# Optimization experiments

Hardware: AMD Instinct MI355X
Metric: run time of the kernel (lower is better)

Reference implementation:

```python
import jax, jax.numpy as jnp
import numpy as np

N = 20000   # atoms
E = 320000  # edges (avg degree 16)
H = 128     # hidden_channels / num_filters
G = 128     # num_gaussians
L = 4       # num_interactions
B = 200     # molecules
V = 80      # _MAX_ATOM_TYPE
CUT = 5.0
LOG2 = float(np.log(2.0))


def setup_inputs() -> dict:
    key = jax.random.key(0)
    ks = jax.random.split(key, 20)
    s = 0.05
    pos = jax.random.uniform(ks[0], (N, 3), dtype=jnp.float32) * 2.5  # dists < 5 = cutoff
    z = jax.random.randint(ks[1], (N,), 0, V)
    batch = jnp.sort(jax.random.randint(ks[2], (N,), 0, B))
    row = jax.random.randint(ks[3], (E,), 0, N)
    off = jax.random.randint(ks[4], (E,), 1, N)
    col = (row + off) % N  # guarantee row != col (no zero distances)
    edge_index = jnp.stack([row, col], axis=0)
    return {
        'pos': pos, 'z': z, 'batch': batch, 'edge_index': edge_index,
        'emb': jax.random.normal(ks[5], (V, H), jnp.float32) * s,
        'mlp_w1': jax.random.normal(ks[6], (L, G, H), jnp.float32) * s,
        'mlp_b1': jnp.zeros((L, H), jnp.float32),
        'mlp_w2': jax.random.normal(ks[7], (L, H, H), jnp.float32) * s,
        'mlp_b2': jnp.zeros((L, H), jnp.float32),
        'conv_lin1_w': jax.random.normal(ks[8], (L, H, H), jnp.float32) * s,
        'conv_lin2_w': jax.random.normal(ks[9], (L, H, H), jnp.float32) * s,
        'conv_lin2_b': jnp.zeros((L, H), jnp.float32),
        'blk_lin_w': jax.random.normal(ks[10], (L, H, H), jnp.float32) * s,
        'blk_lin_b': jnp.zeros((L, H), jnp.float32),
        'head_w1': jax.random.normal(ks[11], (H, H // 2), jnp.float32) * s,
        'head_b1': jnp.zeros((H // 2,), jnp.float32),
        'head_w2': jax.random.normal(ks[12], (H // 2, 1), jnp.float32) * s,
        'head_b2': jnp.zeros((1,), jnp.float32),
    }


def _ssp(x):  # ShiftedSoftplus
    return jax.nn.softplus(x) - LOG2


def _energy(pos, emb, mlp_w1, mlp_b1, mlp_w2, mlp_b2, conv_lin1_w, conv_lin2_w,
            conv_lin2_b, blk_lin_w, blk_lin_b, head_w1, head_b1, head_w2, head_b2,
            z, batch, edge_index):
    row, col = edge_index[0], edge_index[1]
    diff = pos[row] - pos[col]
    d = jnp.sqrt(jnp.sum(diff * diff, axis=-1))  # [E]
    # GaussianSmearing(0, cutoff, G)
    offset = jnp.linspace(0.0, CUT, G, dtype=pos.dtype)
    coeff = -0.5 / (offset[1] - offset[0]) ** 2
    edge_attr = jnp.exp(coeff * (d[:, None] - offset[None, :]) ** 2)  # [E,G]
    Ccut = 0.5 * (jnp.cos(d * jnp.pi / CUT) + 1.0)  # [E]
    h = emb[z]  # [N,H]
    for i in range(L):
        # per-edge filter MLP * cosine cutoff
        W = _ssp(edge_attr @ mlp_w1[i] + mlp_b1[i]) @ mlp_w2[i] + mlp_b2[i]
        W = W * Ccut[:, None]  # [E,H]
        hx = h @ conv_lin1_w[i]  # lin1, no bias
        msg = hx[row] * W  # gather x_j * filter
        agg = jax.ops.segment_sum(msg, col, num_segments=N)  # scatter-add
        v = agg @ conv_lin2_w[i] + conv_lin2_b[i]
        h = h + (_ssp(v) @ blk_lin_w[i] + blk_lin_b[i])  # residual InteractionBlock
    hh = _ssp(h @ head_w1 + head_b1) @ head_w2 + head_b2  # [N,1]
    return jax.ops.segment_sum(hh[:, 0], batch, num_segments=B)  # [B]


def reference(pos, z, batch, edge_index, emb, mlp_w1, mlp_b1, mlp_w2, mlp_b2,
              conv_lin1_w, conv_lin2_w, conv_lin2_b, blk_lin_w, blk_lin_b,
              head_w1, head_b1, head_w2, head_b2):
    args = (emb, mlp_w1, mlp_b1, mlp_w2, mlp_b2, conv_lin1_w, conv_lin2_w,
            conv_lin2_b, blk_lin_w, blk_lin_b, head_w1, head_b1, head_w2, head_b2)
    out = _energy(pos, *args, z, batch, edge_index)
    # forces = -d(sum(energy))/d(pos), matching torch.autograd.grad with ones grad_outputs
    forces = -jax.grad(lambda p: jnp.sum(_energy(p, *args, z, batch, edge_index)))(pos)
    return out, forces
```

## Files before the change

kernel.cpp:

```cpp
#include <hip/hip_runtime.h>

#define HD 128

constexpr int N_ATOMS = 20000;
constexpr int N_EDGES = 320000;
constexpr int NLAY   = 4;
constexpr int NMOL   = 200;
constexpr float FCUT  = 5.0f;
constexpr float DELTA = FCUT / 127.0f;
constexpr float GCOEFF = -0.5f / (DELTA * DELTA);
constexpr float PI_F  = 3.14159265358979323846f;
constexpr float LN2F  = 0.6931471805599453f;

typedef unsigned short u16;
typedef __attribute__((ext_vector_type(8))) short short8v;
typedef __attribute__((ext_vector_type(4))) float f32x4;

__device__ __forceinline__ float sspf(float x) {
  return fmaxf(x, 0.0f) + log1pf(expf(-fabsf(x))) - LN2F;
}
__device__ __forceinline__ float sigmf(float x) {
  return 1.0f / (1.0f + expf(-x));
}

__device__ __forceinline__ unsigned bfpack(float a, float b) {
  unsigned ua = __float_as_uint(a);
  unsigned ub = __float_as_uint(b);
  ua = (ua + 0x7FFFu + ((ua >> 16) & 1u)) >> 16;
  ub = (ub + 0x7FFFu + ((ub >> 16) & 1u)) >> 16;
  return (ub << 16) | ua;
}
__device__ __forceinline__ float bflo(unsigned p) { return __uint_as_float(p << 16); }
__device__ __forceinline__ float bfhi(unsigned p) { return __uint_as_float(p & 0xFFFF0000u); }
__device__ __forceinline__ u16 f2bf(float x) {
  unsigned u = __float_as_uint(x);
  u = (u + 0x7FFFu + ((u >> 16) & 1u)) >> 16;
  return (u16)u;
}
__device__ __forceinline__ float bf2f(u16 b) { return __uint_as_float((unsigned)b << 16); }

__device__ __forceinline__ unsigned packhl(float s) {
  unsigned hs = __float_as_uint(s) & 0xffff0000u;
  float lo = s - __uint_as_float(hs);
  return hs | (__float_as_uint(lo) >> 16);
}

__device__ __forceinline__ unsigned hpair_f32(unsigned a, unsigned b, unsigned& lopair) {
  unsigned ha = a & 0xffff0000u, hb = b & 0xffff0000u;
  float la = __uint_as_float(a) - __uint_as_float(ha);
  float lb = __uint_as_float(b) - __uint_as_float(hb);
  lopair = (__float_as_uint(lb) & 0xffff0000u) | (__float_as_uint(la) >> 16);
  return hb | (ha >> 16);
}


__global__ __launch_bounds__(256) void h0_k(
    const float* __restrict__ emb, const int* __restrict__ z,
    float* __restrict__ h0)
{
  int i = blockIdx.x * 256 + threadIdx.x;
  if (i >= N_ATOMS * HD) return;
  int n = i >> 7, k = i & 127;
  h0[i] = emb[z[n] * HD + k];
}

__global__ __launch_bounds__(256) void wprep_k(
    const float* __restrict__ l1, const float* __restrict__ l2,
    const float* __restrict__ bw, const float* __restrict__ mw1,
    const float* __restrict__ mw2,
    u16* __restrict__ wt, u16* __restrict__ wp, u16* __restrict__ mt)
{
  int i = blockIdx.x * 256 + threadIdx.x;
  if (i >= NLAY * 5 * HD * HD) return;
  int e = i & (HD * HD - 1);
  int wl = i >> 14;
  int wsel = wl % 5;
  int lay = wl / 5;
  const float* W;
  if      (wsel == 0) W = l1;
  else if (wsel == 1) W = l2;
  else if (wsel == 2) W = bw;
  else if (wsel == 3) W = mw1;
  else                W = mw2;
  W += (size_t)lay * HD * HD;
  u16 b = f2bf(W[e]);
  int k = e >> 7, n = e & 127;
  if (wsel < 3) {
    size_t base = (size_t)(lay * 3 + wsel) << 14;
    wp[base + e] = b;
    wt[base + (size_t)n * HD + k] = b;
  } else {
    size_t base = (size_t)(lay * 2 + (wsel - 3)) << 14;
    mt[base + (size_t)n * HD + k] = b;
  }
}

__global__ __launch_bounds__(256) void histboth_k(
    const int* __restrict__ row, const int* __restrict__ col,
    int* __restrict__ cntR, int* __restrict__ cntC)
{
  int e = blockIdx.x * 256 + threadIdx.x;
  if (e >= N_EDGES) return;
  atomicAdd(&cntC[col[e]], 1);
  atomicAdd(&cntR[row[e]], 1);
}

__global__ __launch_bounds__(256) void scan2_k(
    const int* __restrict__ cnt0, const int* __restrict__ cnt1,
    int* __restrict__ cptr, int* __restrict__ rptr,
    int* __restrict__ cur0, int* __restrict__ cur1,
    int* __restrict__ binc, int* __restrict__ binr)
{
  constexpr int CH = 80;
  __shared__ int part[256];
  __shared__ int lh[256];
  const int* cnt = blockIdx.x == 0 ? cnt0 : cnt1;
  int* ptr = blockIdx.x == 0 ? cptr : rptr;
  int* cur = blockIdx.x == 0 ? cur0 : cur1;
  int* bin = blockIdx.x == 0 ? binc : binr;
  int t = threadIdx.x;
  lh[t] = 0;
  int base = t * CH;
  int v[CH];
  if (base + CH <= N_ATOMS) {
#pragma unroll
    for (int i = 0; i < CH / 4; i++) {
      int4 q = *(const int4*)(cnt + base + i * 4);
      v[4*i+0] = q.x; v[4*i+1] = q.y; v[4*i+2] = q.z; v[4*i+3] = q.w;
    }
  } else {
#pragma unroll
    for (int i = 0; i < CH; i++)
      v[i] = (base + i < N_ATOMS) ? cnt[base + i] : 0;
  }
  __syncthreads();
#pragma unroll
  for (int i = 0; i < CH; i++)
    if (base + i < N_ATOMS) atomicAdd(&lh[255 - min(v[i], 255)], 1);
  int s = 0;
#pragma unroll
  for (int i = 0; i < CH; i++) s += v[i];
  part[t] = s;
  __syncthreads();
  bin[t] = lh[t];
  for (int off = 1; off < 256; off <<= 1) {
    int u = (t >= off) ? part[t - off] : 0;
    __syncthreads();
    part[t] += u;
    __syncthreads();
  }
  int run = part[t] - s;
#pragma unroll
  for (int i = 0; i < CH; i++) {
    int idx = base + i;
    if (idx < N_ATOMS) { ptr[idx] = run; cur[idx] = run; }
    else if (idx == N_ATOMS) ptr[idx] = run;
    run += v[i];
  }
}

__global__ __launch_bounds__(256) void scatboth_k(
    const float* __restrict__ pos, const int* __restrict__ row,
    const int* __restrict__ col, int* __restrict__ cur0,
    int* __restrict__ cur1, uint2* __restrict__ cpk2,
    uint2* __restrict__ rpk2, float* __restrict__ cdist,
    float* __restrict__ rdist, int* __restrict__ cslot, float inv_h)
{
  int e = blockIdx.x * 256 + threadIdx.x;
  if (e >= N_EDGES) return;
  int r = row[e], c = col[e];
  float dx = pos[3*r+0] - pos[3*c+0];
  float dy = pos[3*r+1] - pos[3*c+1];
  float dz = pos[3*r+2] - pos[3*c+2];
  float d = sqrtf(dx*dx + dy*dy + dz*dz);
  float fi = d * inv_h;
  int i0 = (int)fi;
  float t = fi - (float)i0;
  unsigned pk = (unsigned)c | ((unsigned)i0 << 16);
  unsigned tu = __float_as_uint(t);
  int pr = atomicAdd(&cur1[r], 1);
  rpk2[pr] = make_uint2(pk, tu);
  rdist[pr] = d;
  int pc = atomicAdd(&cur0[c], 1);
  cpk2[pc] = make_uint2((unsigned)r | ((unsigned)i0 << 16), tu);
  cdist[pc] = d;
  cslot[pc] = pr;
}

__global__ __launch_bounds__(256) void dscan_k(
    int* __restrict__ binc, int* __restrict__ binr)
{
  int* bin = blockIdx.x == 0 ? binc : binr;
  __shared__ int sh[256];
  int t = threadIdx.x;
  int v = bin[t];
  sh[t] = v;
  __syncthreads();
  for (int off = 1; off < 256; off <<= 1) {
    int u = (t >= off) ? sh[t - off] : 0;
    __syncthreads();
    sh[t] += u;
    __syncthreads();
  }
  bin[t] = sh[t] - v;
}

__global__ __launch_bounds__(256) void dscat_k(
    const int* __restrict__ cptr, const int* __restrict__ rptr,
    int* __restrict__ binc, int* __restrict__ binr,
    int* __restrict__ permc, int* __restrict__ permr)
{
  __shared__ int lhc[256], lhr[256], lbc[256], lbr[256];
  int t = threadIdx.x;
  lhc[t] = 0; lhr[t] = 0;
  __syncthreads();
  int a = blockIdx.x * 256 + t;
  int bc = 0, br = 0, rc = 0, rr = 0;
  bool valid = a < N_ATOMS;
  if (valid) {
    int dc = cptr[a+1] - cptr[a];
    int dr = rptr[a+1] - rptr[a];
    bc = 255 - min(dc, 255);
    br = 255 - min(dr, 255);
    rc = atomicAdd(&lhc[bc], 1);
    rr = atomicAdd(&lhr[br], 1);
  }
  __syncthreads();
  if (lhc[t] > 0) lbc[t] = atomicAdd(&binc[t], lhc[t]);
  if (lhr[t] > 0) lbr[t] = atomicAdd(&binr[t], lhr[t]);
  __syncthreads();
  if (valid) {
    permc[lbc[bc] + rc] = a;
    permr[lbr[br] + rr] = a;
  }
}

__global__ __launch_bounds__(256) void nodeA_k(
    float* __restrict__ A, float* __restrict__ dA, int nnode, float hstep)
{
  int i = blockIdx.x * 256 + threadIdx.x;
  if (i >= nnode * HD) return;
  int node = i >> 7, g = i & 127;
  float d = (float)node * hstep;
  float t = d - (float)g * DELTA;
  float a = expf(GCOEFF * t * t);
  A[i] = a;
  dA[i] = a * 2.0f * GCOEFF * t;
}

__global__ __launch_bounds__(256) void nodeact_k(
    const float* __restrict__ t1, const float* __restrict__ u,
    float* __restrict__ s, float* __restrict__ sp, int total)
{
  int i = blockIdx.x * 256 + threadIdx.x;
  if (i >= total) return;
  float x = t1[i];
  s[i] = sspf(x);
  sp[i] = sigmf(x) * u[i];
}

__global__ __launch_bounds__(256) void nodecomb_k(
    const float* __restrict__ P0, const float* __restrict__ D0,
    unsigned* __restrict__ T, int nnode, float hstep)
{
  int i = blockIdx.x * 256 + threadIdx.x;
  int total = NLAY * nnode * HD;
  if (i >= total) return;
  int rem = i % (nnode * HD);
  int node = rem >> 7;
  float d = (float)node * hstep;
  float C  = 0.5f * cosf(d * (PI_F / FCUT)) + 0.5f;
  float Cp = -0.5f * sinf(d * (PI_F / FCUT)) * (PI_F / FCUT);
  float p = P0[i], q = D0[i];
  T[i] = bfpack(p * C, q * C + p * Cp);
}

__device__ __forceinline__ void wave_mm(
    const float* __restrict__ Av, const u16* __restrict__ Bt,
    int m0, int wbase, int lc, int lg, int mclamp, f32x4 acc[2])
{
  short8v bfr[4][2];
#pragma unroll
  for (int ks = 0; ks < 4; ++ks)
#pragma unroll
    for (int nt = 0; nt < 2; ++nt)
      bfr[ks][nt] = *(const short8v*)(Bt + (size_t)(wbase + nt*16 + lc) * HD + ks*32 + lg*8);
  int ar = m0 + lc;
  if (ar > mclamp) ar = mclamp;
  f32x4 z = {0.f, 0.f, 0.f, 0.f};
  acc[0] = z; acc[1] = z;
#pragma unroll
  for (int ks = 0; ks < 4; ++ks) {
    const float* p = Av + (size_t)ar * HD + ks*32 + lg*8;
    uint4 u0 = *(const uint4*)p;
    uint4 u1 = *(const uint4*)(p + 4);
    unsigned p0l, p1l, p2l, p3l;
    unsigned p0h = hpair_f32(u0.x, u0.y, p0l);
    unsigned p1h = hpair_f32(u0.z, u0.w, p1l);
    unsigned p2h = hpair_f32(u1.x, u1.y, p2l);
    unsigned p3h = hpair_f32(u1.z, u1.w, p3l);
    uint4 hv = make_uint4(p0h, p1h, p2h, p3h);
    uint4 lv = make_uint4(p0l, p1l, p2l, p3l);
    short8v ah = *(short8v*)&hv, al = *(short8v*)&lv;
    acc[0] = __builtin_amdgcn_mfma_f32_16x16x32_bf16(ah, bfr[ks][0], acc[0], 0, 0, 0);
    acc[1] = __builtin_amdgcn_mfma_f32_16x16x32_bf16(ah, bfr[ks][1], acc[1], 0, 0, 0);
    acc[0] = __builtin_amdgcn_mfma_f32_16x16x32_bf16(al, bfr[ks][0], acc[0], 0, 0, 0);
    acc[1] = __builtin_amdgcn_mfma_f32_16x16x32_bf16(al, bfr[ks][1], acc[1], 0, 0, 0);
  }
}

__device__ __forceinline__ void wave_mm_lds(
    const unsigned (*__restrict__ Sl)[132], const u16* __restrict__ Bt,
    int wbase, int lc, int lg, f32x4 acc[2])
{
  short8v bfr[4][2];
#pragma unroll
  for (int ks = 0; ks < 4; ++ks)
#pragma unroll
    for (int nt = 0; nt < 2; ++nt)
      bfr[ks][nt] = *(const short8v*)(Bt + (size_t)(wbase + nt*16 + lc) * HD + ks*32 + lg*8);
  f32x4 z = {0.f, 0.f, 0.f, 0.f};
  acc[0] = z; acc[1] = z;
#pragma unroll
  for (int ks = 0; ks < 4; ++ks) {
    uint4 u0 = *(const uint4*)&Sl[lc][ks*32 + lg*8];
    uint4 u1 = *(const uint4*)&Sl[lc][ks*32 + lg*8 + 4];
    uint4 hv = make_uint4(
      (u0.y & 0xffff0000u) | (u0.x >> 16),
      (u0.w & 0xffff0000u) | (u0.z >> 16),
      (u1.y & 0xffff0000u) | (u1.x >> 16),
      (u1.w & 0xffff0000u) | (u1.z >> 16));
    uint4 lv = make_uint4(
      (u0.y << 16) | (u0.x & 0xffffu),
      (u0.w << 16) | (u0.z & 0xffffu),
      (u1.y << 16) | (u1.x & 0xffffu),
      (u1.w << 16) | (u1.z & 0xffffu));
    short8v ah = *(short8v*)&hv, al = *(short8v*)&lv;
    acc[0] = __builtin_amdgcn_mfma_f32_16x16x32_bf16(ah, bfr[ks][0], acc[0], 0, 0, 0);
    acc[1] = __builtin_amdgcn_mfma_f32_16x16x32_bf16(ah, bfr[ks][1], acc[1], 0, 0, 0);
    acc[0] = __builtin_amdgcn_mfma_f32_16x16x32_bf16(al, bfr[ks][0], acc[0], 0, 0, 0);
    acc[1] = __builtin_amdgcn_mfma_f32_16x16x32_bf16(al, bfr[ks][1], acc[1], 0, 0, 0);
  }
}

__global__ __launch_bounds__(256) void nmm_hx_k(
    const float* __restrict__ h, const u16* __restrict__ Bt,
    u16* __restrict__ hx, int M)
{
  int t = threadIdx.x, lane = t & 63;
  int lc = lane & 15, lg = lane >> 4;
  int wbase = (t >> 6) * 32;
  int m0 = blockIdx.x * 16;
  f32x4 acc[2];
  wave_mm(h, Bt, m0, wbase, lc, lg, M - 1, acc);
#pragma unroll
  for (int nt = 0; nt < 2; ++nt) {
    int ccol = wbase + nt*16 + lc;
#pragma unroll
    for (int j = 0; j < 4; ++j) {
      int grow = m0 + lg*4 + j;
      if (grow < M) hx[(size_t)grow * HD + ccol] = f2bf(acc[nt][j]);
    }
  }
}

__global__ __launch_bounds__(256) void nmm_bwdT_k(
    const float* __restrict__ A, const u16* __restrict__ Bp,
    const float* __restrict__ addin, float* __restrict__ C, int M)
{
  int t = threadIdx.x, lane = t & 63;
  int lc = lane & 15, lg = lane >> 4;
  int wbase = (t >> 6) * 32;
  int m0 = blockIdx.x * 16;
  f32x4 acc[2];
  wave_mm(A, Bp, m0, wbase, lc, lg, M - 1, acc);
#pragma unroll
  for (int nt = 0; nt < 2; ++nt) {
    int ccol = wbase + nt*16 + lc;
#pragma unroll
    for (int j = 0; j < 4; ++j) {
      int grow = m0 + lg*4 + j;
      if (grow < M)
        C[(size_t)grow * HD + ccol] = acc[nt][j] + addin[(size_t)grow * HD + ccol];
    }
  }
}

__global__ __launch_bounds__(256) void ftail_f_k(
    const float* __restrict__ agg, const u16* __restrict__ l2t,
    const float* __restrict__ l2b, const u16* __restrict__ bwt,
    const float* __restrict__ bb, const float* __restrict__ h,
    u16* __restrict__ svb, float* __restrict__ hout,
    const u16* __restrict__ l1n, u16* __restrict__ hxn, int M)
{
  __shared__ unsigned Sl[16][132];
  int t = threadIdx.x, lane = t & 63;
  int lc = lane & 15, lg = lane >> 4;
  int wbase = (t >> 6) * 32;
  int m0 = blockIdx.x * 16;
  f32x4 acc[2];
  wave_mm(agg, l2t, m0, wbase, lc, lg, M - 1, acc);
#pragma unroll
  for (int nt = 0; nt < 2; ++nt) {
    int ccol = wbase + nt*16 + lc;
    float bv = l2b[ccol];
#pragma unroll
    for (int j = 0; j < 4; ++j) {
      int lrow = lg*4 + j;
      int grow = m0 + lrow;
      float s = 0.0f;
      if (grow < M) {
        float x = acc[nt][j] + bv;
        svb[(size_t)grow * HD + ccol] = f2bf(sigmf(x));
        s = sspf(x);
      }
      Sl[lrow][ccol] = packhl(s);
    }
  }
  __syncthreads();
  wave_mm_lds(Sl, bwt, wbase, lc, lg, acc);

  float ho[2][4];
#pragma unroll
  for (int nt = 0; nt < 2; ++nt) {
    int ccol = wbase + nt*16 + lc;
    float bv = bb[ccol];
#pragma unroll
    for (int j = 0; j < 4; ++j) {
      int grow = m0 + lg*4 + j;
      float x = 0.0f;
      if (grow < M) {
        x = acc[nt][j] + bv + h[(size_t)grow * HD + ccol];
        hout[(size_t)grow * HD + ccol] = x;
      }
      ho[nt][j] = x;
    }
  }
  if (l1n) {
    __syncthreads();
#pragma unroll
    for (int nt = 0; nt < 2; ++nt) {
      int ccol = wbase + nt*16 + lc;
#pragma unroll
      for (int j = 0; j < 4; ++j)
        Sl[lg*4 + j][ccol] = packhl(ho[nt][j]);
    }
    __syncthreads();
    wave_mm_lds(Sl, l1n, wbase, lc, lg, acc);
#pragma unroll
    for (int nt = 0; nt < 2; ++nt) {
      int ccol = wbase + nt*16 + lc;
#pragma unroll
      for (int j = 0; j < 4; ++j) {
        int grow = m0 + lg*4 + j;
        if (grow < M) hxn[(size_t)grow * HD + ccol] = f2bf(acc[nt][j]);
      }
    }
  }
}

__global__ __launch_bounds__(256) void bhead_f_k(
    const float* __restrict__ g, const u16* __restrict__ bwp,
    const u16* __restrict__ svb, const u16* __restrict__ l2p,
    u16* __restrict__ dagg, int M)
{
  __shared__ unsigned Sl[16][132];
  int t = threadIdx.x, lane = t & 63;
  int lc = lane & 15, lg = lane >> 4;
  int wbase = (t >> 6) * 32;
  int m0 = blockIdx.x * 16;
  f32x4 acc[2];
  wave_mm(g, bwp, m0, wbase, lc, lg, M - 1, acc);
#pragma unroll
  for (int nt = 0; nt < 2; ++nt) {
    int ccol = wbase + nt*16 + lc;
#pragma unroll
    for (int j = 0; j < 4; ++j) {
      int lrow = lg*4 + j;
      int grow = m0 + lrow;
      float dv = 0.0f;
      if (grow < M)
        dv = acc[nt][j] * bf2f(svb[(size_t)grow * HD + ccol]);
      Sl[lrow][ccol] = packhl(dv);
    }
  }
  __syncthreads();
  wave_mm_lds(Sl, l2p, wbase, lc, lg, acc);
#pragma unroll
  for (int nt = 0; nt < 2; ++nt) {
    int ccol = wbase + nt*16 + lc;
#pragma unroll
    for (int j = 0; j < 4; ++j) {
      int grow = m0 + lg*4 + j;
      if (grow < M) dagg[(size_t)grow * HD + ccol] = f2bf(acc[nt][j]);
    }
  }
}

__global__ __launch_bounds__(256) void tblmm2_k(
    const float* __restrict__ A0, const float* __restrict__ A1, size_t astride,
    const u16* __restrict__ Bt, size_t bstride,
    const float* __restrict__ bias0, size_t biasstride,
    float* __restrict__ C0, float* __restrict__ C1, size_t cstride, int M)
{
  int l = blockIdx.y;
  int zz = blockIdx.z;
  const float* A = (zz ? A1 : A0) + (size_t)l * astride;
  const u16* B = Bt + (size_t)l * bstride;
  const float* bias = zz ? nullptr : (bias0 ? bias0 + (size_t)l * biasstride : nullptr);
  float* C = (zz ? C1 : C0) + (size_t)l * cstride;
  int t = threadIdx.x, lane = t & 63;
  int lc = lane & 15, lg = lane >> 4;
  int wbase = (t >> 6) * 32;
  int m0 = blockIdx.x * 16;
  f32x4 acc[2];
  wave_mm(A, B, m0, wbase, lc, lg, M - 1, acc);
#pragma unroll
  for (int nt = 0; nt < 2; ++nt) {
    int ccol = wbase + nt*16 + lc;
    float bv = bias ? bias[ccol] : 0.0f;
#pragma unroll
    for (int j = 0; j < 4; ++j) {
      int grow = m0 + lg*4 + j;
      if (grow < M) C[(size_t)grow * HD + ccol] = acc[nt][j] + bv;
    }
  }
}

__global__ __launch_bounds__(256) void gath_fwd_k(
    const int* __restrict__ perm, const int* __restrict__ cptr,
    const uint2* __restrict__ cpk2, const unsigned* __restrict__ T,
    const unsigned* __restrict__ hx, float* __restrict__ agg, float hstep)
{
  int ai = blockIdx.x * 4 + (threadIdx.x >> 6);
  if (ai >= N_ATOMS) return;
  int a = perm[ai];
  int half = (threadIdx.x >> 5) & 1;
  int l32 = threadIdx.x & 31;
  int ch = l32 * 4;
  int beg = cptr[a], end = cptr[a + 1];
  float s0 = 0.f, s1 = 0.f, s2 = 0.f, s3 = 0.f;
#pragma unroll 2
  for (int j = beg + half; j < end; j += 2) {
    uint2 pk2 = cpk2[j];
    float t = __uint_as_float(pk2.y);
    int other = pk2.x & 0xffffu;
    float t2 = t * t, t3 = t2 * t;
    float cx = 2.f*t3 - 3.f*t2 + 1.f;
    float cy = (t3 - 2.f*t2 + t) * hstep;
    float cz = 3.f*t2 - 2.f*t3;
    float cw = (t3 - t2) * hstep;
    const unsigned* tp = T + (size_t)(pk2.x >> 16) * HD + ch;
    uint4 q0 = *(const uint4*)(tp);
    uint4 q1 = *(const uint4*)(tp + HD);
    uint2 hp = *(const uint2*)(hx + (size_t)other * 64 + l32 * 2);
    float v0 = cx*bflo(q0.x) + cy*bfhi(q0.x) + cz*bflo(q1.x) + cw*bfhi(q1.x);
    float v1 = cx*bflo(q0.y) + cy*bfhi(q0.y) + cz*bflo(q1.y) + cw*bfhi(q1.y);
    float v2 = cx*bflo(q0.z) + cy*bfhi(q0.z) + cz*bflo(q1.z) + cw*bfhi(q1.z);
    float v3 = cx*bflo(q0.w) + cy*bfhi(q0.w) + cz*bflo(q1.w) + cw*bfhi(q1.w);
    s0 = fmaf(bflo(hp.x), v0, s0);
    s1 = fmaf(bfhi(hp.x), v1, s1);
    s2 = fmaf(bflo(hp.y), v2, s2);
    s3 = fmaf(bfhi(hp.y), v3, s3);
  }
  s0 += __shfl_xor(s0, 32, 64);
  s1 += __shfl_xor(s1, 32, 64);
  s2 += __shfl_xor(s2, 32, 64);
  s3 += __shfl_xor(s3, 32, 64);
  if (half == 0)
    *(float4*)(agg + (size_t)a * HD + ch) = make_float4(s0, s1, s2, s3);
}

__global__ __launch_bounds__(256) void gath_bwd_k(
    const int* __restrict__ perm, const int* __restrict__ rptr,
    const uint2* __restrict__ rpk2, const unsigned* __restrict__ T,
    const unsigned* __restrict__ dagg, const unsigned* __restrict__ hx,
    float* __restrict__ dhx, float* __restrict__ ddslot, int accum,
    float hstep, float inv_h)
{
  int ai = blockIdx.x * 4 + (threadIdx.x >> 6);
  if (ai >= N_ATOMS) return;
  int a = perm[ai];
  int half = (threadIdx.x >> 5) & 1;
  int l32 = threadIdx.x & 31;
  int ch = l32 * 4;
  int beg = rptr[a], end = rptr[a + 1];
  uint2 hp = *(const uint2*)(hx + (size_t)a * 64 + l32 * 2);
  float h0 = bflo(hp.x), h1 = bfhi(hp.x), h2 = bflo(hp.y), h3 = bfhi(hp.y);
  float s0 = 0.f, s1 = 0.f, s2 = 0.f, s3 = 0.f;
#pragma unroll 2
  for (int j = beg + half; j < end; j += 2) {
    uint2 pk2 = rpk2[j];
    float t = __uint_as_float(pk2.y);
    int other = pk2.x & 0xffffu;
    float t2 = t * t, t3 = t2 * t;
    float cax = 2.f*t3 - 3.f*t2 + 1.f;
    float cay = (t3 - 2.f*t2 + t) * hstep;
    float caz = 3.f*t2 - 2.f*t3;
    float caw = (t3 - t2) * hstep;
    float cbx = (6.f*t2 - 6.f*t) * inv_h;
    float cby = 3.f*t2 - 4.f*t + 1.f;
    float cbz = -cbx;
    float cbw = 3.f*t2 - 2.f*t;
    const unsigned* tp = T + (size_t)(pk2.x >> 16) * HD + ch;
    uint4 q0 = *(const uint4*)(tp);
    uint4 q1 = *(const uint4*)(tp + HD);
    uint2 dp = *(const uint2*)(dagg + (size_t)other * 64 + l32 * 2);
    float da0 = bflo(dp.x), da1 = bfhi(dp.x), da2 = bflo(dp.y), da3 = bfhi(dp.y);
    float x0l = bflo(q0.x), x0h = bfhi(q0.x), y0l = bflo(q1.x), y0h = bfhi(q1.x);
    float x1l = bflo(q0.y), x1h = bfhi(q0.y), y1l = bflo(q1.y), y1h = bfhi(q1.y);
    float x2l = bflo(q0.z), x2h = bfhi(q0.z), y2l = bflo(q1.z), y2h = bfhi(q1.z);
    float x3l = bflo(q0.w), x3h = bfhi(q0.w), y3l = bflo(q1.w), y3h = bfhi(q1.w);
    float v0 = cax*x0l + cay*x0h + caz*y0l + caw*y0h;
    float v1 = cax*x1l + cay*x1h + caz*y1l + caw*y1h;
    float v2 = cax*x2l + cay*x2h + caz*y2l + caw*y2h;
    float v3 = cax*x3l + cay*x3h + caz*y3l + caw*y3h;
    float g0 = cbx*x0l + cby*x0h + cbz*y0l + cbw*y0h;
    float g1 = cbx*x1l + cby*x1h + cbz*y1l + cbw*y1h;
    float g2 = cbx*x2l + cby*x2h + cbz*y2l + cbw*y2h;
    float g3 = cbx*x3l + cby*x3h + cbz*y3l + cbw*y3h;
    s0 = fmaf(da0, v0, s0);
    s1 = fmaf(da1, v1, s1);
    s2 = fmaf(da2, v2, s2);
    s3 = fmaf(da3, v3, s3);
    float dot = da0*h0*g0 + da1*h1*g1 + da2*h2*g2 + da3*h3*g3;
#pragma unroll
    for (int off = 16; off > 0; off >>= 1) dot += __shfl_down(dot, off, 32);
    if (l32 == 0) ddslot[j] = accum ? (ddslot[j] + dot) : dot;
  }
  s0 += __shfl_xor(s0, 32, 64);
  s1 += __shfl_xor(s1, 32, 64);
  s2 += __shfl_xor(s2, 32, 64);
  s3 += __shfl_xor(s3, 32, 64);
  if (half == 0)
    *(float4*)(dhx + (size_t)a * HD + ch) = make_float4(s0, s1, s2, s3);
}

__global__ __launch_bounds__(256) void headf_k(
    const float* __restrict__ h4, const float* __restrict__ hw1,
    const float* __restrict__ hb1, const float* __restrict__ hw2,
    const float* __restrict__ hb2, float* __restrict__ ea,
    float* __restrict__ gh)
{
  __shared__ float As[16][68];
  __shared__ float Bs[16][132];
  __shared__ float Ss[64][68];
  __shared__ float red[64][17];
  int t = threadIdx.x;
  int tx = t & 15, ty = t >> 4;
  int m0 = blockIdx.x * 64;

  float acc4[4][4];
#pragma unroll
  for (int r = 0; r < 4; r++)
#pragma unroll
    for (int c = 0; c < 4; c++) acc4[r][c] = 0.0f;

  for (int k0 = 0; k0 < HD; k0 += 16) {
    {
      int rrow = t >> 2;
      int kg = (t & 3) * 4;
      int gm = m0 + rrow;
      float4 av = make_float4(0.f, 0.f, 0.f, 0.f);
      if (gm < N_ATOMS) av = *(const float4*)(h4 + (size_t)gm * HD + k0 + kg);
      As[kg+0][rrow] = av.x; As[kg+1][rrow] = av.y;
      As[kg+2][rrow] = av.z; As[kg+3][rrow] = av.w;
    }
    if (t < 256) {
      int kk = t >> 4;
      int n4 = (t & 15) * 4;
      float4 bv = *(const float4*)(hw1 + (size_t)(k0 + kk) * 64 + n4);
      *(float4*)&Bs[kk][n4] = bv;
    }
    __syncthreads();
#pragma unroll
    for (int kk = 0; kk < 16; kk++) {
      float a[4], b[4];
#pragma unroll
      for (int r = 0; r < 4; r++) a[r] = As[kk][ty * 4 + r];
#pragma unroll
      for (int c = 0; c < 4; c++) b[c] = Bs[kk][tx * 4 + c];
#pragma unroll
      for (int r = 0; r < 4; r++)
#pragma unroll
        for (int c = 0; c < 4; c++) acc4[r][c] = fmaf(a[r], b[c], acc4[r][c]);
    }
    __syncthreads();
  }

  {
    int n0 = tx * 4;
    float b1v[4], w2v[4];
#pragma unroll
    for (int c = 0; c < 4; c++) { b1v[c] = hb1[n0 + c]; w2v[c] = hw2[n0 + c]; }
#pragma unroll
    for (int r = 0; r < 4; r++) {
      int lr = ty * 4 + r;
      float p = 0.0f;
#pragma unroll
      for (int c = 0; c < 4; c++) {
        float x = acc4[r][c] + b1v[c];
        p += sspf(x) * w2v[c];
        Ss[lr][n0 + c] = sigmf(x) * w2v[c];
      }
      red[lr][tx] = p;
    }
  }
  __syncthreads();
  if (t < 64) {
    int gm = m0 + t;
    if (gm < N_ATOMS) {
      float s = hb2[0];
#pragma unroll
      for (int j = 0; j < 16; j++) s += red[t][j];
      ea[gm] = s;
    }
  }

  float acc[4][8];
#pragma unroll
  for (int r = 0; r < 4; r++)
#pragma unroll
    for (int c = 0; c < 8; c++) acc[r][c] = 0.0f;

  for (int j0 = 0; j0 < 64; j0 += 16) {
#pragma unroll
    for (int it = 0; it < 2; it++) {
      int idx = t + it * 256;
      int n = idx >> 2;
      int jg = (idx & 3) * 4;
      float4 bv = *(const float4*)(hw1 + (size_t)n * 64 + j0 + jg);
      Bs[jg+0][n] = bv.x; Bs[jg+1][n] = bv.y;
      Bs[jg+2][n] = bv.z; Bs[jg+3][n] = bv.w;
    }
    __syncthreads();
#pragma unroll
    for (int kk = 0; kk < 16; kk++) {
      float a[4], b[8];
#pragma unroll
      for (int r = 0; r < 4; r++) a[r] = Ss[ty * 4 + r][j0 + kk];
#pragma unroll
      for (int c = 0; c < 8; c++) b[c] = Bs[kk][tx * 8 + c];
#pragma unroll
      for (int r = 0; r < 4; r++)
#pragma unroll
        for (int c = 0; c < 8; c++) acc[r][c] = fmaf(a[r], b[c], acc[r][c]);
    }
    __syncthreads();
  }

  int n0 = tx * 8;
#pragma unroll
  for (int r = 0; r < 4; r++) {
    int gm = m0 + ty * 4 + r;
    if (gm >= N_ATOMS) continue;
    *(float4*)(gh + (size_t)gm * HD + n0)     = *(float4*)&acc[r][0];
    *(float4*)(gh + (size_t)gm * HD + n0 + 4) = *(float4*)&acc[r][4];
  }
}

__global__ __launch_bounds__(64) void ered_k(
    const int* __restrict__ batch, const float* __restrict__ ea,
    float* __restrict__ energy)
{
  int m = blockIdx.x;
  int lo = 0, hi = N_ATOMS;
  while (lo < hi) { int mid = (lo + hi) >> 1; if (batch[mid] < m) lo = mid + 1; else hi = mid; }
  int beg = lo;
  lo = beg; hi = N_ATOMS;
  while (lo < hi) { int mid = (lo + hi) >> 1; if (batch[mid] < m + 1) lo = mid + 1; else hi = mid; }
  int end = lo;
  float s = 0.0f;
  for (int i = beg + threadIdx.x; i < end; i += 64) s += ea[i];
#pragma unroll
  for (int off = 32; off > 0; off >>= 1) s += __shfl_down(s, off, 64);
  if (threadIdx.x == 0) energy[m] = s;
}

__global__ __launch_bounds__(256) void forceg_k(
    const int* __restrict__ rptr, const uint2* __restrict__ rpk2,
    const float* __restrict__ rdist,
    const int* __restrict__ cptr, const uint2* __restrict__ cpk2,
    const float* __restrict__ cdist, const int* __restrict__ cslot,
    const float* __restrict__ ddslot, const float* __restrict__ pos,
    float* __restrict__ force)
{
  int idx = blockIdx.x * 256 + threadIdx.x;
  int a = idx >> 3;
  int g = idx & 7;
  if (a >= N_ATOMS) return;
  float px = pos[3*a+0], py = pos[3*a+1], pz = pos[3*a+2];
  float fx = 0.f, fy = 0.f, fz = 0.f;
  int beg = rptr[a], end = rptr[a+1];
  for (int j = beg + g; j < end; j += 8) {
    int o = rpk2[j].x & 0xffffu;
    float w = ddslot[j] / rdist[j];
    fx -= w * (px - pos[3*o+0]);
    fy -= w * (py - pos[3*o+1]);
    fz -= w * (pz - pos[3*o+2]);
  }
  beg = cptr[a]; end = cptr[a+1];
  for (int j = beg + g; j < end; j += 8) {
    int o = cpk2[j].x & 0xffffu;
    float w = ddslot[cslot[j]] / cdist[j];
    fx -= w * (px - pos[3*o+0]);
    fy -= w * (py - pos[3*o+1]);
    fz -= w * (pz - pos[3*o+2]);
  }
#pragma unroll
  for (int off = 4; off > 0; off >>= 1) {
    fx += __shfl_down(fx, off, 8);
    fy += __shfl_down(fy, off, 8);
    fz += __shfl_down(fz, off, 8);
  }
  if (g == 0) {
    force[3*a+0] = fx;
    force[3*a+1] = fy;
    force[3*a+2] = fz;
  }
}

static inline int nblk(int m) { return (m + 63) / 64; }

extern "C" void kernel_launch(void* const* d_in, const int* in_sizes, int n_in,
                              void* d_out, int out_size, void* d_ws, size_t ws_size,
                              hipStream_t stream)
{
  const float* pos   = (const float*)d_in[0];
  const int*   z     = (const int*)d_in[1];
  const int*   batch = (const int*)d_in[2];
  const int*   eidx  = (const int*)d_in[3];
  const float* emb   = (const float*)d_in[4];
  const float* mlp_w1 = (const float*)d_in[5];
  const float* mlp_b1 = (const float*)d_in[6];
  const float* mlp_w2 = (const float*)d_in[7];
  const float* mlp_b2 = (const float*)d_in[8];
  const float* lin1_w = (const float*)d_in[9];
  const float* lin2_w = (const float*)d_in[10];
  const float* lin2_b = (const float*)d_in[11];
  const float* blk_w  = (const float*)d_in[12];
  const float* blk_b  = (const float*)d_in[13];
  const float* hw1 = (const float*)d_in[14];
  const float* hb1 = (const float*)d_in[15];
  const float* hw2 = (const float*)d_in[16];
  const float* hb2 = (const float*)d_in[17];

  float* out = (float*)d_out;
  float* ws  = (float*)d_ws;

  const int* row = eidx;
  const int* col = eidx + N_EDGES;

  const size_t NH = (size_t)N_ATOMS * HD;
  size_t o = 0;
  float* ddslot = ws + o; o += N_EDGES;
  int* cptr = (int*)(ws + o); o += N_ATOMS + 1;
  int* rptr = (int*)(ws + o); o += N_ATOMS + 1;
  int* cnt0 = (int*)(ws + o); o += N_ATOMS;
  int* cnt1 = (int*)(ws + o); o += N_ATOMS;
  int* binc = (int*)(ws + o); o += 256;
  int* binr = (int*)(ws + o); o += 256;
  int* cur0 = (int*)(ws + o); o += N_ATOMS;
  int* cur1 = (int*)(ws + o); o += N_ATOMS;
  int* permc = (int*)(ws + o); o += N_ATOMS;
  int* permr = (int*)(ws + o); o += N_ATOMS;
  int* cslot = (int*)(ws + o); o += N_EDGES;
  float* cdist = ws + o; o += N_EDGES;
  float* rdist = ws + o; o += N_EDGES;
  o = (o + 1) & ~(size_t)1;
  uint2* cpk2 = (uint2*)(ws + o); o += (size_t)2 * N_EDGES;
  uint2* rpk2 = (uint2*)(ws + o); o += (size_t)2 * N_EDGES;
  u16* wt = (u16*)(ws + o); o += (size_t)NLAY * 3 * HD * HD / 2;
  u16* wp = (u16*)(ws + o); o += (size_t)NLAY * 3 * HD * HD / 2;
  u16* mt = (u16*)(ws + o); o += (size_t)NLAY * 2 * HD * HD / 2;
  float* hxb[4];
  for (int i = 0; i < 4; i++) { hxb[i] = ws + o; o += NH / 2; }
  float* svb[4];
  for (int i = 0; i < 4; i++) { svb[i] = ws + o; o += NH / 2; }
  float* hA  = ws + o; o += NH;
  float* hB  = ws + o; o += NH;
  float* agg = ws + o; o += NH;
  float* g0b = ws + o; o += NH;
  float* g1b = ws + o; o += NH;
  float* dgb = ws + o; o += NH / 2;

  int NT = 1024;
  while (NT > 128) {
    size_t need = o + (size_t)NLAY * (NT + 1) * HD;
    if (need * sizeof(float) <= ws_size) break;
    NT >>= 1;
  }
  const int NN = NT + 1;
  const float hstep = FCUT / (float)NT;
  const float inv_h = (float)NT / FCUT;
  unsigned* T = (unsigned*)(ws + o); o += (size_t)NLAY * NN * HD;

  const int EB = (N_EDGES + 255) / 256;
  const int ABK = (N_ATOMS + 255) / 256;

  hipMemsetAsync(cnt0, 0, 2 * N_ATOMS * sizeof(int), stream);

  wprep_k<<<(NLAY * 5 * HD * HD + 255) / 256, 256, 0, stream>>>(
      lin1_w, lin2_w, blk_w, mlp_w1, mlp_w2, wt, wp, mt);

  histboth_k<<<EB, 256, 0, stream>>>(row, col, cnt1, cnt0);
  scan2_k<<<2, 256, 0, stream>>>(cnt0, cnt1, cptr, rptr, cur0, cur1, binc, binr);
  scatboth_k<<<EB, 256, 0, stream>>>(pos, row, col, cur0, cur1, cpk2, rpk2,
                                     cdist, rdist, cslot, inv_h);

  dscan_k<<<2, 256, 0, stream>>>(binc, binr);
  dscat_k<<<ABK, 256, 0, stream>>>(cptr, rptr, binc, binr, permc, permr);

  {
    const size_t LNH = (size_t)NN * HD;
    float* Anode  = agg;
    float* dAnode = agg + LNH;
    float* t1 = dgb;
    float* u  = g0b;
    float* s  = g1b;
    float* sp = hA;
    nodeA_k<<<((int)LNH + 255) / 256, 256, 0, stream>>>(Anode, dAnode, NN, hstep);
    dim3 gB16((NN + 15) / 16, NLAY, 2);
    tblmm2_k<<<gB16, 256, 0, stream>>>(Anode, dAnode, 0, mt, 32768,
                                       mlp_b1, HD, t1, u, LNH, NN);
    int tot = (int)(NLAY * LNH);
    nodeact_k<<<(tot + 255) / 256, 256, 0, stream>>>(t1, u, s, sp, tot);
    float* P0 = dgb;
    float* D0 = g0b;
    tblmm2_k<<<gB16, 256, 0, stream>>>(s, sp, LNH, mt + 16384, 32768,
                                       mlp_b2, HD, P0, D0, LNH, NN);
    nodecomb_k<<<(tot + 255) / 256, 256, 0, stream>>>(P0, D0, T, NN, hstep);
  }

  h0_k<<<(N_ATOMS * HD + 255) / 256, 256, 0, stream>>>(emb, z, hA);

  const int AB = (N_ATOMS + 3) / 4;
  const int GB = nblk(N_ATOMS);
  const int NB16 = (N_ATOMS + 15) / 16;

  float* hcur = hA;
  float* hnxt = hB;
  nmm_hx_k<<<NB16, 256, 0, stream>>>(hcur, wt, (u16*)hxb[0], N_ATOMS);
  for (int i = 0; i < NLAY; i++) {
    const u16* l2t = wt + ((size_t)(i*3 + 1) << 14);
    const u16* bwt = wt + ((size_t)(i*3 + 2) << 14);
    const u16* l1n = (i < NLAY - 1) ? wt + ((size_t)((i+1)*3 + 0) << 14) : nullptr;
    u16* hxn = (i < NLAY - 1) ? (u16*)hxb[i+1] : nullptr;
    const float* l2bi = lin2_b + (size_t)i * HD;
    const float* bbi  = blk_b + (size_t)i * HD;
    const unsigned* Tl = T + (size_t)i * NN * HD;

    gath_fwd_k<<<AB, 256, 0, stream>>>(permc, cptr, cpk2, Tl,
                                       (const unsigned*)hxb[i], agg, hstep);
    ftail_f_k<<<NB16, 256, 0, stream>>>(agg, l2t, l2bi, bwt, bbi, hcur,
                                        (u16*)svb[i], hnxt, l1n, hxn, N_ATOMS);
    float* tmp = hcur; hcur = hnxt; hnxt = tmp;
  }

  float* ea = dgb;
  headf_k<<<GB, 256, 0, stream>>>(hcur, hw1, hb1, hw2, hb2, ea, g0b);
  ered_k<<<NMOL, 64, 0, stream>>>(batch, ea, out);

  float* gcur = g0b;
  float* gnxt = g1b;
  for (int i = NLAY - 1; i >= 0; i--) {
    const u16* l1p = wp + ((size_t)(i*3 + 0) << 14);
    const u16* l2p = wp + ((size_t)(i*3 + 1) << 14);
    const u16* bwp = wp + ((size_t)(i*3 + 2) << 14);
    const unsigned* Tl = T + (size_t)i * NN * HD;

    bhead_f_k<<<NB16, 256, 0, stream>>>(gcur, bwp, (const u16*)svb[i], l2p,
                                        (u16*)dgb, N_ATOMS);
    gath_bwd_k<<<AB, 256, 0, stream>>>(permr, rptr, rpk2, Tl,
                                       (const unsigned*)dgb,
                                       (const unsigned*)hxb[i], agg, ddslot,
                                       i != NLAY - 1, hstep, inv_h);
    if (i > 0) {
      nmm_bwdT_k<<<NB16, 256, 0, stream>>>(agg, l1p, gcur, gnxt, N_ATOMS);
      float* tmp = gcur; gcur = gnxt; gnxt = tmp;
    }
  }

  forceg_k<<<(N_ATOMS * 8 + 255) / 256, 256, 0, stream>>>(
      rptr, rpk2, rdist, cptr, cpk2, cdist, cslot, ddslot, pos, out + NMOL);
}
```

Before: 768.1 us.

## Fuse backward lin1-transpose GEMM into next block head kernel; skip unused dhx

The separate nmm_bwdT kernel, which computed the hidden gradient from the aggregated dhx, is folded into the next layer's bhead kernel. That kernel now does the lin1-transpose GEMM plus residual add, stages the result in LDS and runs the blk-lin GEMM from there, which removes a launch and a global round trip of the gradient. The layer-0 gather-backward also skips the unused dhx accumulation and its spline coefficients, since no downstream consumer needs it. In exchange the fused kernel adds an extra GEMM stage and syncs per block, and still writes gout when a later layer needs it.

Measured after the change: 763.3 us. About the same (-0.6%).

```diff
diff --git a/kernel.cpp b/kernel.cpp
--- a/kernel.cpp
+++ b/kernel.cpp
@@ -364,28 +364,6 @@
   }
 }
 
-__global__ __launch_bounds__(256) void nmm_bwdT_k(
-    const float* __restrict__ A, const u16* __restrict__ Bp,
-    const float* __restrict__ addin, float* __restrict__ C, int M)
-{
-  int t = threadIdx.x, lane = t & 63;
-  int lc = lane & 15, lg = lane >> 4;
-  int wbase = (t >> 6) * 32;
-  int m0 = blockIdx.x * 16;
-  f32x4 acc[2];
-  wave_mm(A, Bp, m0, wbase, lc, lg, M - 1, acc);
-#pragma unroll
-  for (int nt = 0; nt < 2; ++nt) {
-    int ccol = wbase + nt*16 + lc;
-#pragma unroll
-    for (int j = 0; j < 4; ++j) {
-      int grow = m0 + lg*4 + j;
-      if (grow < M)
-        C[(size_t)grow * HD + ccol] = acc[nt][j] + addin[(size_t)grow * HD + ccol];
-    }
-  }
-}
-
 __global__ __launch_bounds__(256) void ftail_f_k(
     const float* __restrict__ agg, const u16* __restrict__ l2t,
     const float* __restrict__ l2b, const u16* __restrict__ bwt,
@@ -459,10 +437,12 @@
   }
 }
 
-__global__ __launch_bounds__(256) void bhead_f_k(
-    const float* __restrict__ g, const u16* __restrict__ bwp,
-    const u16* __restrict__ svb, const u16* __restrict__ l2p,
-    u16* __restrict__ dagg, int M)
+__global__ __launch_bounds__(256) void bhead2_f_k(
+    const float* __restrict__ aggprev, const u16* __restrict__ l1prev,
+    const float* __restrict__ gadd, const float* __restrict__ gdirect,
+    const u16* __restrict__ bwp, const u16* __restrict__ svb,
+    const u16* __restrict__ l2p, u16* __restrict__ dagg,
+    float* __restrict__ gout, int M)
 {
   __shared__ unsigned Sl[16][132];
   int t = threadIdx.x, lane = t & 63;
@@ -470,7 +450,29 @@
   int wbase = (t >> 6) * 32;
   int m0 = blockIdx.x * 16;
   f32x4 acc[2];
-  wave_mm(g, bwp, m0, wbase, lc, lg, M - 1, acc);
+  if (aggprev) {
+    wave_mm(aggprev, l1prev, m0, wbase, lc, lg, M - 1, acc);
+#pragma unroll
+    for (int nt = 0; nt < 2; ++nt) {
+      int ccol = wbase + nt*16 + lc;
+#pragma unroll
+      for (int j = 0; j < 4; ++j) {
+        int lrow = lg*4 + j;
+        int grow = m0 + lrow;
+        float x = 0.0f;
+        if (grow < M) {
+          x = acc[nt][j] + gadd[(size_t)grow * HD + ccol];
+          if (gout) gout[(size_t)grow * HD + ccol] = x;
+        }
+        Sl[lrow][ccol] = packhl(x);
+      }
+    }
+    __syncthreads();
+    wave_mm_lds(Sl, bwp, wbase, lc, lg, acc);
+    __syncthreads();
+  } else {
+    wave_mm(gdirect, bwp, m0, wbase, lc, lg, M - 1, acc);
+  }
 #pragma unroll
   for (int nt = 0; nt < 2; ++nt) {
     int ccol = wbase + nt*16 + lc;
@@ -576,7 +578,7 @@
     const uint2* __restrict__ rpk2, const unsigned* __restrict__ T,
     const unsigned* __restrict__ dagg, const unsigned* __restrict__ hx,
     float* __restrict__ dhx, float* __restrict__ ddslot, int accum,
-    float hstep, float inv_h)
+    int need_dhx, float hstep, float inv_h)
 {
   int ai = blockIdx.x * 4 + (threadIdx.x >> 6);
   if (ai >= N_ATOMS) return;
@@ -594,10 +596,6 @@
     float t = __uint_as_float(pk2.y);
     int other = pk2.x & 0xffffu;
     float t2 = t * t, t3 = t2 * t;
-    float cax = 2.f*t3 - 3.f*t2 + 1.f;
-    float cay = (t3 - 2.f*t2 + t) * hstep;
-    float caz = 3.f*t2 - 2.f*t3;
-    float caw = (t3 - t2) * hstep;
     float cbx = (6.f*t2 - 6.f*t) * inv_h;
     float cby = 3.f*t2 - 4.f*t + 1.f;
     float cbz = -cbx;
@@ -611,29 +609,41 @@
     float x1l = bflo(q0.y), x1h = bfhi(q0.y), y1l = bflo(q1.y), y1h = bfhi(q1.y);
     float x2l = bflo(q0.z), x2h = bfhi(q0.z), y2l = bflo(q1.z), y2h = bfhi(q1.z);
     float x3l = bflo(q0.w), x3h = bfhi(q0.w), y3l = bflo(q1.w), y3h = bfhi(q1.w);
-    float v0 = cax*x0l + cay*x0h + caz*y0l + caw*y0h;
-    float v1 = cax*x1l + cay*x1h + caz*y1l + caw*y1h;
-    float v2 = cax*x2l + cay*x2h + caz*y2l + caw*y2h;
-    float v3 = cax*x3l + cay*x3h + caz*y3l + caw*y3h;
     float g0 = cbx*x0l + cby*x0h + cbz*y0l + cbw*y0h;
     float g1 = cbx*x1l + cby*x1h + cbz*y1l + cbw*y1h;
     float g2 = cbx*x2l + cby*x2h + cbz*y2l + cbw*y2h;
     float g3 = cbx*x3l + cby*x3h + cbz*y3l + cbw*y3h;
-    s0 = fmaf(da0, v0, s0);
-    s1 = fmaf(da1, v1, s1);
-    s2 = fmaf(da2, v2, s2);
-    s3 = fmaf(da3, v3, s3);
-    float dot = da0*h0*g0 + da1*h1*g1 + da2*h2*g2 + da3*h3*g3;
+    float dah0 = da0*h0, dah1 = da1*h1, dah2 = da2*h2, dah3 = da3*h3;
+    float dot = dah0*g0;
+    dot = fmaf(dah1, g1, dot);
+    dot = fmaf(dah2, g2, dot);
+    dot = fmaf(dah3, g3, dot);
 #pragma unroll
     for (int off = 16; off > 0; off >>= 1) dot += __shfl_down(dot, off, 32);
     if (l32 == 0) ddslot[j] = accum ? (ddslot[j] + dot) : dot;
-  }
-  s0 += __shfl_xor(s0, 32, 64);
-  s1 += __shfl_xor(s1, 32, 64);
-  s2 += __shfl_xor(s2, 32, 64);
-  s3 += __shfl_xor(s3, 32, 64);
-  if (half == 0)
-    *(float4*)(dhx + (size_t)a * HD + ch) = make_float4(s0, s1, s2, s3);
+    if (need_dhx) {
+      float cax = 2.f*t3 - 3.f*t2 + 1.f;
+      float cay = (t3 - 2.f*t2 + t) * hstep;
+      float caz = 3.f*t2 - 2.f*t3;
+      float caw = (t3 - t2) * hstep;
+      float v0 = cax*x0l + cay*x0h + caz*y0l + caw*y0h;
+      float v1 = cax*x1l + cay*x1h + caz*y1l + caw*y1h;
+      float v2 = cax*x2l + cay*x2h + caz*y2l + caw*y2h;
+      float v3 = cax*x3l + cay*x3h + caz*y3l + caw*y3h;
+      s0 = fmaf(da0, v0, s0);
+      s1 = fmaf(da1, v1, s1);
+      s2 = fmaf(da2, v2, s2);
+      s3 = fmaf(da3, v3, s3);
+    }
+  }
+  if (need_dhx) {
+    s0 += __shfl_xor(s0, 32, 64);
+    s1 += __shfl_xor(s1, 32, 64);
+    s2 += __shfl_xor(s2, 32, 64);
+    s3 += __shfl_xor(s3, 32, 64);
+    if (half == 0)
+      *(float4*)(dhx + (size_t)a * HD + ch) = make_float4(s0, s1, s2, s3);
+  }
 }
 
 __global__ __launch_bounds__(256) void headf_k(
@@ -964,21 +974,26 @@
   float* gcur = g0b;
   float* gnxt = g1b;
   for (int i = NLAY - 1; i >= 0; i--) {
-    const u16* l1p = wp + ((size_t)(i*3 + 0) << 14);
     const u16* l2p = wp + ((size_t)(i*3 + 1) << 14);
     const u16* bwp = wp + ((size_t)(i*3 + 2) << 14);
     const unsigned* Tl = T + (size_t)i * NN * HD;
 
-    bhead_f_k<<<NB16, 256, 0, stream>>>(gcur, bwp, (const u16*)svb[i], l2p,
-                                        (u16*)dgb, N_ATOMS);
+    if (i == NLAY - 1) {
+      bhead2_f_k<<<NB16, 256, 0, stream>>>(nullptr, nullptr, nullptr, gcur,
+                                           bwp, (const u16*)svb[i], l2p,
+                                           (u16*)dgb, nullptr, N_ATOMS);
+    } else {
+      const u16* l1nx = wp + ((size_t)((i+1)*3 + 0) << 14);
+      float* gout = (i > 0) ? gnxt : nullptr;
+      bhead2_f_k<<<NB16, 256, 0, stream>>>(agg, l1nx, gcur, nullptr,
+                                           bwp, (const u16*)svb[i], l2p,
+                                           (u16*)dgb, gout, N_ATOMS);
+      if (i > 0) { float* tmp = gcur; gcur = gnxt; gnxt = tmp; }
+    }
     gath_bwd_k<<<AB, 256, 0, stream>>>(permr, rptr, rpk2, Tl,
                                        (const unsigned*)dgb,
                                        (const unsigned*)hxb[i], agg, ddslot,
-                                       i != NLAY - 1, hstep, inv_h);
-    if (i > 0) {
-      nmm_bwdT_k<<<NB16, 256, 0, stream>>>(agg, l1p, gcur, gnxt, N_ATOMS);
-      float* tmp = gcur; gcur = gnxt; gnxt = tmp;
-    }
+                                       i != NLAY - 1, i != 0, hstep, inv_h);
   }
 
   forceg_k<<<(N_ATOMS * 8 + 255) / 256, 256, 0, stream>>>(
```
